# Kernel tuning notes

Hardware: AMD Instinct MI355X
Metric: run time of the kernel (lower is better)

The kernel has to match this reference:

```python
import jax, jax.numpy as jnp
import numpy as np

N_NODES = 5000
N_EDGES = 160000
HID = 64
NODE_F = 4
TASK_F = 4
BATCH = 512


def _glorot(key, shape):
    fan_in = shape[-1]
    return jax.random.normal(key, shape, dtype=jnp.float32) / jnp.sqrt(jnp.float32(fan_in))


def setup_inputs() -> dict:
    key = jax.random.key(0)
    ks = jax.random.split(key, 16)
    x = jax.random.normal(ks[0], (N_NODES, NODE_F), dtype=jnp.float32)
    edge_index = jax.random.randint(ks[1], (2, N_EDGES), 0, N_NODES, dtype=jnp.int64)
    task_feat = jax.random.normal(ks[2], (BATCH, TASK_F), dtype=jnp.float32)
    return {
        "x": x,
        "edge_index": edge_index,
        "task_feat": task_feat,
        # SAGEConv layer 1: out = lin_l(mean_neigh) + lin_r(x); lin_l has bias, lin_r (root) has no bias (PyG default)
        "Wl1": _glorot(ks[3], (HID, NODE_F)), "bl1": jnp.zeros((HID,), jnp.float32),
        "Wr1": _glorot(ks[4], (HID, NODE_F)),
        # SAGEConv layer 2
        "Wl2": _glorot(ks[5], (HID, HID)), "bl2": jnp.zeros((HID,), jnp.float32),
        "Wr2": _glorot(ks[6], (HID, HID)),
        # task_encoder: Linear(4,64) -> ReLU -> Linear(64,64)
        "Wt1": _glorot(ks[7], (HID, TASK_F)), "bt1": jnp.zeros((HID,), jnp.float32),
        "Wt2": _glorot(ks[8], (HID, HID)), "bt2": jnp.zeros((HID,), jnp.float32),
        # classifier: Linear(128,64) -> ReLU -> Linear(64,1)
        "Wc1": _glorot(ks[9], (HID, 2 * HID)), "bc1": jnp.zeros((HID,), jnp.float32),
        "Wc2": _glorot(ks[10], (1, HID)), "bc2": jnp.zeros((1,), jnp.float32),
    }


def _sage_conv(x, src, dst, Wl, bl, Wr):
    # PyG SAGEConv(mean): messages flow src -> dst; mean over incoming neighbors
    msg_sum = jax.ops.segment_sum(x[src], dst, num_segments=N_NODES)
    deg = jax.ops.segment_sum(jnp.ones((src.shape[0],), x.dtype), dst, num_segments=N_NODES)
    mean_neigh = msg_sum / jnp.maximum(deg, 1.0)[:, None]
    return mean_neigh @ Wl.T + bl + x @ Wr.T


def reference(x, edge_index, task_feat,
              Wl1, bl1, Wr1, Wl2, bl2, Wr2,
              Wt1, bt1, Wt2, bt2, Wc1, bc1, Wc2, bc2):
    src, dst = edge_index[0], edge_index[1]
    h = jax.nn.relu(_sage_conv(x, src, dst, Wl1, bl1, Wr1))        # [N, HID]
    h = jax.nn.relu(_sage_conv(h, src, dst, Wl2, bl2, Wr2))        # [N, HID]
    t = jax.nn.relu(task_feat @ Wt1.T + bt1) @ Wt2.T + bt2         # [B, HID]
    # classifier on concat([h, t]) == split Wc1 into h-part and t-part; avoids materializing the concat
    h_part = h @ Wc1[:, :HID].T                                    # [N, HID]
    t_part = t @ Wc1[:, HID:].T + bc1                              # [B, HID]
    hidden = jax.nn.relu(h_part[None, :, :] + t_part[:, None, :])  # [B, N, HID]
    scores = jnp.einsum('bnh,h->bn', hidden, Wc2[0]) + bc2[0]      # [B, N]
    return scores
```

## Files before the change

kernel.cpp:

```cpp
#include <hip/hip_runtime.h>

#define N_NODES 5000
#define N_EDGES 160000
#define HID 64
#define BATCH 512
#define EPB 2500
#define STRIDE 256


__global__ __launch_bounds__(256) void prep_kernel(
        const int* __restrict__ ei,
        const float* __restrict__ Wl1, const float* __restrict__ Wr1,
        const float* __restrict__ Wl2, const float* __restrict__ Wr2,
        const float* __restrict__ Wc1,
        const float* __restrict__ task_feat,
        const float* __restrict__ Wt1, const float* __restrict__ bt1,
        const float* __restrict__ Wt2, const float* __restrict__ bt2,
        const float* __restrict__ bc1,
        int* __restrict__ blk_hist,
        float* __restrict__ Wl1T, float* __restrict__ Wr1T,
        float* __restrict__ Wl2T, float* __restrict__ Wr2T,
        float* __restrict__ Wc1hT, float* __restrict__ t_part) {
    int tid = threadIdx.x;
    int blk = blockIdx.x;
    __shared__ int hist[N_NODES];
    __shared__ float s1[4][64], s2[4][64];

    if (blk < 64) {
        for (int i = tid; i < N_NODES; i += 256) hist[i] = 0;
        __syncthreads();
        int base = blk * EPB;
        for (int j = tid; j < EPB; j += 256)
            atomicAdd(&hist[ei[N_EDGES + base + j]], 1);
        __syncthreads();
        for (int i = tid; i < N_NODES; i += 256)
            blk_hist[blk * N_NODES + i] = hist[i];
    } else if (blk == 64) {
        for (int idx = tid; idx < 4096; idx += 256) {
            int k = idx >> 6, h = idx & 63;
            Wl2T[idx] = Wl2[h * 64 + k];
        }
    } else if (blk == 65) {
        for (int idx = tid; idx < 4096; idx += 256) {
            int k = idx >> 6, h = idx & 63;
            Wr2T[idx] = Wr2[h * 64 + k];
        }
    } else if (blk == 66) {
        for (int idx = tid; idx < 4096; idx += 256) {
            int k = idx >> 6, h = idx & 63;
            Wc1hT[idx] = Wc1[h * 128 + k];
        }
    } else if (blk == 67) {
        int k = tid >> 6, h = tid & 63;
        Wl1T[tid] = Wl1[h * 4 + k];
        Wr1T[tid] = Wr1[h * 4 + k];
    } else {
        int grp = tid >> 6, h = tid & 63;
        int b = (blk - 68) * 4 + grp;
        float4 tf = ((const float4*)task_feat)[b];
        float4 w1 = ((const float4*)Wt1)[h];
        float v = bt1[h] + tf.x * w1.x + tf.y * w1.y + tf.z * w1.z + tf.w * w1.w;
        s1[grp][h] = fmaxf(v, 0.f);
        __syncthreads();
        const float4* w2r = (const float4*)(Wt2 + h * 64);
        const float4* s1v = (const float4*)s1[grp];
        float v2 = bt2[h];
#pragma unroll
        for (int q = 0; q < 16; q++) {
            float4 w = w2r[q]; float4 s = s1v[q];
            v2 += s.x * w.x + s.y * w.y + s.z * w.z + s.w * w.w;
        }
        s2[grp][h] = v2;
        __syncthreads();
        const float4* wc  = (const float4*)(Wc1 + h * 128 + 64);
        const float4* s2v = (const float4*)s2[grp];
        float p = bc1[h];
#pragma unroll
        for (int q = 0; q < 16; q++) {
            float4 w = wc[q]; float4 s = s2v[q];
            p += s.x * w.x + s.y * w.y + s.z * w.z + s.w * w.w;
        }
        t_part[b * 64 + h] = p;
    }
}

__global__ __launch_bounds__(256) void offsets_kernel(int* __restrict__ blk_hist,
                                                      int* __restrict__ deg) {
    int n = blockIdx.x * 256 + threadIdx.x;
    if (n >= N_NODES) return;
    int run = 0;
#pragma unroll 8
    for (int b = 0; b < 64; b++) {
        int v = blk_hist[b * N_NODES + n];
        blk_hist[b * N_NODES + n] = run;
        run += v;
    }
    deg[n] = run;
}

__global__ __launch_bounds__(256) void reorder_kernel(
        const int* __restrict__ ei, const int* __restrict__ blk_hist,
        int* __restrict__ sorted_src) {
    __shared__ int cur[N_NODES];
    int tid = threadIdx.x;
    int blk = blockIdx.x;
    for (int i = tid; i < N_NODES; i += 256) cur[i] = 0;
    __syncthreads();
    int base = blk * EPB;
    const int* my_excl = blk_hist + blk * N_NODES;
    for (int j = tid; j < EPB; j += 256) {
        int src = ei[base + j];
        int dst = ei[N_EDGES + base + j];
        int local = atomicAdd(&cur[dst], 1);
        sorted_src[dst * STRIDE + my_excl[dst] + local] = src;
    }
}

__global__ __launch_bounds__(256) void layer1_kernel(
        const float* __restrict__ x, const int* __restrict__ deg,
        const int* __restrict__ sorted_src,
        const float* __restrict__ Wl1T, const float* __restrict__ bl1,
        const float* __restrict__ Wr1T, float* __restrict__ h1) {
    int lane = threadIdx.x & 63, grp = threadIdx.x >> 6;
    int n = blockIdx.x * 4 + grp;
    int d = deg[n];
    int f = lane & 3, g = lane >> 2;
    const int* bucket = sorted_src + n * STRIDE;
    float acc = 0.f;
    for (int j = g; j < d; j += 16) acc += x[bucket[j] * 4 + f];
    acc += __shfl_down(acc, 32);
    acc += __shfl_down(acc, 16);
    acc += __shfl_down(acc, 8);
    acc += __shfl_down(acc, 4);
    __shared__ float mean[4][4], xn[4][4];
    if (lane < 4) {
        mean[grp][lane] = acc / fmaxf((float)d, 1.f);
        xn[grp][lane] = x[n * 4 + lane];
    }
    __syncthreads();
    float v = bl1[lane];
#pragma unroll
    for (int ff = 0; ff < 4; ff++)
        v += mean[grp][ff] * Wl1T[ff * 64 + lane] + xn[grp][ff] * Wr1T[ff * 64 + lane];
    h1[n * 64 + lane] = fmaxf(v, 0.f);
}

__global__ __launch_bounds__(256) void layer2_kernel(
        const float* __restrict__ h1, const int* __restrict__ deg,
        const int* __restrict__ sorted_src,
        const float* __restrict__ Wl2T, const float* __restrict__ bl2,
        const float* __restrict__ Wr2T, const float* __restrict__ Wc1hT,
        float* __restrict__ h_part) {
    int h = threadIdx.x & 63, grp = threadIdx.x >> 6;
    int n = blockIdx.x * 4 + grp;
    int d = deg[n];
    const int* bucket = sorted_src + n * STRIDE;
    float a0 = 0.f, a1 = 0.f, a2 = 0.f, a3 = 0.f;
    int j = 0;
    for (; j + 4 <= d; j += 4) {
        int e0 = bucket[j], e1 = bucket[j + 1], e2 = bucket[j + 2], e3 = bucket[j + 3];
        a0 += h1[e0 * 64 + h];
        a1 += h1[e1 * 64 + h];
        a2 += h1[e2 * 64 + h];
        a3 += h1[e3 * 64 + h];
    }
    for (; j < d; j++) a0 += h1[bucket[j] * 64 + h];
    float m = (a0 + a1 + a2 + a3) / fmaxf((float)d, 1.f);

    __shared__ float shm[4][64], shh[4][64], shh2[4][64];
    shm[grp][h] = m;
    shh[grp][h] = h1[n * 64 + h];
    __syncthreads();
    float v = bl2[h];
#pragma unroll
    for (int k = 0; k < 64; k++)
        v += shm[grp][k] * Wl2T[k * 64 + h] + shh[grp][k] * Wr2T[k * 64 + h];
    shh2[grp][h] = fmaxf(v, 0.f);
    __syncthreads();
    float p = 0.f;
#pragma unroll
    for (int k = 0; k < 64; k++) p += shh2[grp][k] * Wc1hT[k * 64 + h];
    h_part[n * 64 + h] = p;
}

__global__ __launch_bounds__(256) void scores_kernel(
        const float* __restrict__ h_part, const float* __restrict__ t_part,
        const float* __restrict__ Wc2, const float* __restrict__ bc2,
        float* __restrict__ out) {
    int tid = threadIdx.x;
    int n = blockIdx.x * 256 + tid;
    bool valid = n < N_NODES;
    int nn = valid ? n : (N_NODES - 1);
    float hr[64];
    const float4* hp = (const float4*)(h_part + nn * 64);
#pragma unroll
    for (int i = 0; i < 16; i++) {
        float4 v = hp[i];
        hr[4 * i + 0] = v.x; hr[4 * i + 1] = v.y;
        hr[4 * i + 2] = v.z; hr[4 * i + 3] = v.w;
    }
    float b2 = bc2[0];
    int b0 = blockIdx.y * 16;
    for (int bb = 0; bb < 16; bb++) {
        const float* tp = t_part + (b0 + bb) * 64;
        float acc = 0.f;
#pragma unroll
        for (int h = 0; h < 64; h++)
            acc = fmaf(fmaxf(hr[h] + tp[h], 0.f), Wc2[h], acc);
        if (valid) out[(b0 + bb) * N_NODES + n] = acc + b2;
    }
}

extern "C" void kernel_launch(void* const* d_in, const int* in_sizes, int n_in,
                              void* d_out, int out_size, void* d_ws, size_t ws_size,
                              hipStream_t stream) {
    const float* x    = (const float*)d_in[0];
    const int*   ei   = (const int*)d_in[1];
    const float* task = (const float*)d_in[2];
    const float* Wl1  = (const float*)d_in[3];
    const float* bl1  = (const float*)d_in[4];
    const float* Wr1  = (const float*)d_in[5];
    const float* Wl2  = (const float*)d_in[6];
    const float* bl2  = (const float*)d_in[7];
    const float* Wr2  = (const float*)d_in[8];
    const float* Wt1  = (const float*)d_in[9];
    const float* bt1  = (const float*)d_in[10];
    const float* Wt2  = (const float*)d_in[11];
    const float* bt2  = (const float*)d_in[12];
    const float* Wc1  = (const float*)d_in[13];
    const float* bc1  = (const float*)d_in[14];
    const float* Wc2  = (const float*)d_in[15];
    const float* bc2  = (const float*)d_in[16];
    float* out = (float*)d_out;

    char* ws = (char*)d_ws;
    int*   blk_hist   = (int*)(ws + 0);
    int*   deg        = (int*)(ws + 1280000);
    int*   sorted_src = (int*)(ws + 1300000);
    float* h1         = (float*)(ws + 6420000);
    float* h_part     = (float*)(ws + 7700000);
    float* t_part     = (float*)(ws + 8980000);
    float* Wl1T  = (float*)(ws + 9111072);
    float* Wr1T  = (float*)(ws + 9112096);
    float* Wl2T  = (float*)(ws + 9113120);
    float* Wr2T  = (float*)(ws + 9129504);
    float* Wc1hT = (float*)(ws + 9145888);

    prep_kernel<<<68 + BATCH / 4, 256, 0, stream>>>(ei, Wl1, Wr1, Wl2, Wr2, Wc1,
                                                    task, Wt1, bt1, Wt2, bt2, bc1,
                                                    blk_hist, Wl1T, Wr1T, Wl2T, Wr2T,
                                                    Wc1hT, t_part);
    offsets_kernel<<<(N_NODES + 255) / 256, 256, 0, stream>>>(blk_hist, deg);
    reorder_kernel<<<64, 256, 0, stream>>>(ei, blk_hist, sorted_src);
    layer1_kernel<<<N_NODES / 4, 256, 0, stream>>>(x, deg, sorted_src, Wl1T, bl1, Wr1T, h1);
    layer2_kernel<<<N_NODES / 4, 256, 0, stream>>>(h1, deg, sorted_src, Wl2T, bl2, Wr2T,
                                                   Wc1hT, h_part);
    scores_kernel<<<dim3(20, 32), 256, 0, stream>>>(h_part, t_part, Wc2, bc2, out);
}
```

Baseline: 154.6 us.

## Fuse all stages into one cooperative persistent kernel with grid syncs

```diff
diff --git a/kernel.cpp b/kernel.cpp
--- a/kernel.cpp
+++ b/kernel.cpp
@@ -1,259 +1,263 @@
 #include <hip/hip_runtime.h>
+#include <hip/hip_cooperative_groups.h>
+
+namespace cg = cooperative_groups;
 
 #define N_NODES 5000
 #define N_EDGES 160000
 #define HID 64
 #define BATCH 512
-#define EPB 2500
+#define NSLICE 128
+#define EPB (N_EDGES / NSLICE)
 #define STRIDE 256
-
-
-__global__ __launch_bounds__(256) void prep_kernel(
-        const int* __restrict__ ei,
-        const float* __restrict__ Wl1, const float* __restrict__ Wr1,
-        const float* __restrict__ Wl2, const float* __restrict__ Wr2,
-        const float* __restrict__ Wc1,
-        const float* __restrict__ task_feat,
-        const float* __restrict__ Wt1, const float* __restrict__ bt1,
-        const float* __restrict__ Wt2, const float* __restrict__ bt2,
-        const float* __restrict__ bc1,
-        int* __restrict__ blk_hist,
-        float* __restrict__ Wl1T, float* __restrict__ Wr1T,
-        float* __restrict__ Wl2T, float* __restrict__ Wr2T,
-        float* __restrict__ Wc1hT, float* __restrict__ t_part) {
-    int tid = threadIdx.x;
-    int blk = blockIdx.x;
-    __shared__ int hist[N_NODES];
-    __shared__ float s1[4][64], s2[4][64];
-
-    if (blk < 64) {
-        for (int i = tid; i < N_NODES; i += 256) hist[i] = 0;
+#define MAXGRID 640
+
+
+struct Params {
+    const float *x; const int *ei; const float *task;
+    const float *Wl1, *bl1, *Wr1, *Wl2, *bl2, *Wr2;
+    const float *Wt1, *bt1, *Wt2, *bt2, *Wc1, *bc1, *Wc2, *bc2;
+    float *out;
+    int *blk_hist; int *deg; int *sorted_src;
+    float *h1, *h_part, *t_part;
+    float *Wl1T, *Wr1T, *Wl2T, *Wr2T, *Wc1hT;
+};
+
+__global__ __launch_bounds__(256, 2) void fused_kernel(Params p) {
+    cg::grid_group grid = cg::this_grid();
+    const int tid = threadIdx.x;
+    const int nblk = gridDim.x;
+    __shared__ union SM {
+        int   ldsi[N_NODES];
+        float s[3][4][64];
+    } sm;
+
+    for (int u = blockIdx.x; u < NSLICE + 4 + BATCH / 4; u += nblk) {
+        if (u < NSLICE) {
+            for (int i = tid; i < N_NODES; i += 256) sm.ldsi[i] = 0;
+            __syncthreads();
+            int base = u * EPB;
+            for (int j = tid; j < EPB; j += 256)
+                atomicAdd(&sm.ldsi[p.ei[N_EDGES + base + j]], 1);
+            __syncthreads();
+            for (int i = tid; i < N_NODES; i += 256)
+                p.blk_hist[u * N_NODES + i] = sm.ldsi[i];
+        } else if (u < NSLICE + 4) {
+            int w = u - NSLICE;
+            if (w == 0) {
+                for (int idx = tid; idx < 4096; idx += 256) {
+                    int k = idx >> 6, h = idx & 63;
+                    p.Wl2T[idx] = p.Wl2[h * 64 + k];
+                }
+            } else if (w == 1) {
+                for (int idx = tid; idx < 4096; idx += 256) {
+                    int k = idx >> 6, h = idx & 63;
+                    p.Wr2T[idx] = p.Wr2[h * 64 + k];
+                }
+            } else if (w == 2) {
+                for (int idx = tid; idx < 4096; idx += 256) {
+                    int k = idx >> 6, h = idx & 63;
+                    p.Wc1hT[idx] = p.Wc1[h * 128 + k];
+                }
+            } else {
+                int k = tid >> 6, h = tid & 63;
+                p.Wl1T[tid] = p.Wl1[h * 4 + k];
+                p.Wr1T[tid] = p.Wr1[h * 4 + k];
+            }
+        } else {
+            int grp = tid >> 6, h = tid & 63;
+            int b = (u - (NSLICE + 4)) * 4 + grp;
+            float4 tf = ((const float4*)p.task)[b];
+            float4 w1 = ((const float4*)p.Wt1)[h];
+            float v = p.bt1[h] + tf.x * w1.x + tf.y * w1.y + tf.z * w1.z + tf.w * w1.w;
+            sm.s[0][grp][h] = fmaxf(v, 0.f);
+            __syncthreads();
+            const float4* w2r = (const float4*)(p.Wt2 + h * 64);
+            const float4* s1v = (const float4*)sm.s[0][grp];
+            float v2 = p.bt2[h];
+#pragma unroll
+            for (int q = 0; q < 16; q++) {
+                float4 w = w2r[q]; float4 s = s1v[q];
+                v2 += s.x * w.x + s.y * w.y + s.z * w.z + s.w * w.w;
+            }
+            sm.s[1][grp][h] = v2;
+            __syncthreads();
+            const float4* wc  = (const float4*)(p.Wc1 + h * 128 + 64);
+            const float4* s2v = (const float4*)sm.s[1][grp];
+            float pr = p.bc1[h];
+#pragma unroll
+            for (int q = 0; q < 16; q++) {
+                float4 w = wc[q]; float4 s = s2v[q];
+                pr += s.x * w.x + s.y * w.y + s.z * w.z + s.w * w.w;
+            }
+            p.t_part[b * 64 + h] = pr;
+        }
         __syncthreads();
-        int base = blk * EPB;
-        for (int j = tid; j < EPB; j += 256)
-            atomicAdd(&hist[ei[N_EDGES + base + j]], 1);
+    }
+    grid.sync();
+
+    for (int n = blockIdx.x * 256 + tid; n < N_NODES; n += nblk * 256) {
+        int run = 0;
+#pragma unroll 8
+        for (int b = 0; b < NSLICE; b++) {
+            int v = p.blk_hist[b * N_NODES + n];
+            p.blk_hist[b * N_NODES + n] = run;
+            run += v;
+        }
+        p.deg[n] = run;
+    }
+    grid.sync();
+
+    for (int u = blockIdx.x; u < NSLICE; u += nblk) {
+        for (int i = tid; i < N_NODES; i += 256) sm.ldsi[i] = 0;
         __syncthreads();
-        for (int i = tid; i < N_NODES; i += 256)
-            blk_hist[blk * N_NODES + i] = hist[i];
-    } else if (blk == 64) {
-        for (int idx = tid; idx < 4096; idx += 256) {
-            int k = idx >> 6, h = idx & 63;
-            Wl2T[idx] = Wl2[h * 64 + k];
-        }
-    } else if (blk == 65) {
-        for (int idx = tid; idx < 4096; idx += 256) {
-            int k = idx >> 6, h = idx & 63;
-            Wr2T[idx] = Wr2[h * 64 + k];
-        }
-    } else if (blk == 66) {
-        for (int idx = tid; idx < 4096; idx += 256) {
-            int k = idx >> 6, h = idx & 63;
-            Wc1hT[idx] = Wc1[h * 128 + k];
-        }
-    } else if (blk == 67) {
-        int k = tid >> 6, h = tid & 63;
-        Wl1T[tid] = Wl1[h * 4 + k];
-        Wr1T[tid] = Wr1[h * 4 + k];
-    } else {
-        int grp = tid >> 6, h = tid & 63;
-        int b = (blk - 68) * 4 + grp;
-        float4 tf = ((const float4*)task_feat)[b];
-        float4 w1 = ((const float4*)Wt1)[h];
-        float v = bt1[h] + tf.x * w1.x + tf.y * w1.y + tf.z * w1.z + tf.w * w1.w;
-        s1[grp][h] = fmaxf(v, 0.f);
+        int base = u * EPB;
+        const int* excl = p.blk_hist + u * N_NODES;
+        for (int j = tid; j < EPB; j += 256) {
+            int src = p.ei[base + j];
+            int dst = p.ei[N_EDGES + base + j];
+            int local = atomicAdd(&sm.ldsi[dst], 1);
+            p.sorted_src[dst * STRIDE + excl[dst] + local] = src;
+        }
         __syncthreads();
-        const float4* w2r = (const float4*)(Wt2 + h * 64);
-        const float4* s1v = (const float4*)s1[grp];
-        float v2 = bt2[h];
-#pragma unroll
-        for (int q = 0; q < 16; q++) {
-            float4 w = w2r[q]; float4 s = s1v[q];
-            v2 += s.x * w.x + s.y * w.y + s.z * w.z + s.w * w.w;
-        }
-        s2[grp][h] = v2;
-        __syncthreads();
-        const float4* wc  = (const float4*)(Wc1 + h * 128 + 64);
-        const float4* s2v = (const float4*)s2[grp];
-        float p = bc1[h];
-#pragma unroll
-        for (int q = 0; q < 16; q++) {
-            float4 w = wc[q]; float4 s = s2v[q];
-            p += s.x * w.x + s.y * w.y + s.z * w.z + s.w * w.w;
-        }
-        t_part[b * 64 + h] = p;
-    }
-}
-
-__global__ __launch_bounds__(256) void offsets_kernel(int* __restrict__ blk_hist,
-                                                      int* __restrict__ deg) {
-    int n = blockIdx.x * 256 + threadIdx.x;
-    if (n >= N_NODES) return;
-    int run = 0;
-#pragma unroll 8
-    for (int b = 0; b < 64; b++) {
-        int v = blk_hist[b * N_NODES + n];
-        blk_hist[b * N_NODES + n] = run;
-        run += v;
-    }
-    deg[n] = run;
-}
-
-__global__ __launch_bounds__(256) void reorder_kernel(
-        const int* __restrict__ ei, const int* __restrict__ blk_hist,
-        int* __restrict__ sorted_src) {
-    __shared__ int cur[N_NODES];
-    int tid = threadIdx.x;
-    int blk = blockIdx.x;
-    for (int i = tid; i < N_NODES; i += 256) cur[i] = 0;
-    __syncthreads();
-    int base = blk * EPB;
-    const int* my_excl = blk_hist + blk * N_NODES;
-    for (int j = tid; j < EPB; j += 256) {
-        int src = ei[base + j];
-        int dst = ei[N_EDGES + base + j];
-        int local = atomicAdd(&cur[dst], 1);
-        sorted_src[dst * STRIDE + my_excl[dst] + local] = src;
-    }
-}
-
-__global__ __launch_bounds__(256) void layer1_kernel(
-        const float* __restrict__ x, const int* __restrict__ deg,
-        const int* __restrict__ sorted_src,
-        const float* __restrict__ Wl1T, const float* __restrict__ bl1,
-        const float* __restrict__ Wr1T, float* __restrict__ h1) {
-    int lane = threadIdx.x & 63, grp = threadIdx.x >> 6;
-    int n = blockIdx.x * 4 + grp;
-    int d = deg[n];
-    int f = lane & 3, g = lane >> 2;
-    const int* bucket = sorted_src + n * STRIDE;
-    float acc = 0.f;
-    for (int j = g; j < d; j += 16) acc += x[bucket[j] * 4 + f];
-    acc += __shfl_down(acc, 32);
-    acc += __shfl_down(acc, 16);
-    acc += __shfl_down(acc, 8);
-    acc += __shfl_down(acc, 4);
-    __shared__ float mean[4][4], xn[4][4];
-    if (lane < 4) {
-        mean[grp][lane] = acc / fmaxf((float)d, 1.f);
-        xn[grp][lane] = x[n * 4 + lane];
-    }
-    __syncthreads();
-    float v = bl1[lane];
-#pragma unroll
-    for (int ff = 0; ff < 4; ff++)
-        v += mean[grp][ff] * Wl1T[ff * 64 + lane] + xn[grp][ff] * Wr1T[ff * 64 + lane];
-    h1[n * 64 + lane] = fmaxf(v, 0.f);
-}
-
-__global__ __launch_bounds__(256) void layer2_kernel(
-        const float* __restrict__ h1, const int* __restrict__ deg,
-        const int* __restrict__ sorted_src,
-        const float* __restrict__ Wl2T, const float* __restrict__ bl2,
-        const float* __restrict__ Wr2T, const float* __restrict__ Wc1hT,
-        float* __restrict__ h_part) {
-    int h = threadIdx.x & 63, grp = threadIdx.x >> 6;
-    int n = blockIdx.x * 4 + grp;
-    int d = deg[n];
-    const int* bucket = sorted_src + n * STRIDE;
-    float a0 = 0.f, a1 = 0.f, a2 = 0.f, a3 = 0.f;
-    int j = 0;
-    for (; j + 4 <= d; j += 4) {
-        int e0 = bucket[j], e1 = bucket[j + 1], e2 = bucket[j + 2], e3 = bucket[j + 3];
-        a0 += h1[e0 * 64 + h];
-        a1 += h1[e1 * 64 + h];
-        a2 += h1[e2 * 64 + h];
-        a3 += h1[e3 * 64 + h];
-    }
-    for (; j < d; j++) a0 += h1[bucket[j] * 64 + h];
-    float m = (a0 + a1 + a2 + a3) / fmaxf((float)d, 1.f);
-
-    __shared__ float shm[4][64], shh[4][64], shh2[4][64];
-    shm[grp][h] = m;
-    shh[grp][h] = h1[n * 64 + h];
-    __syncthreads();
-    float v = bl2[h];
-#pragma unroll
-    for (int k = 0; k < 64; k++)
-        v += shm[grp][k] * Wl2T[k * 64 + h] + shh[grp][k] * Wr2T[k * 64 + h];
-    shh2[grp][h] = fmaxf(v, 0.f);
-    __syncthreads();
-    float p = 0.f;
-#pragma unroll
-    for (int k = 0; k < 64; k++) p += shh2[grp][k] * Wc1hT[k * 64 + h];
-    h_part[n * 64 + h] = p;
-}
-
-__global__ __launch_bounds__(256) void scores_kernel(
-        const float* __restrict__ h_part, const float* __restrict__ t_part,
-        const float* __restrict__ Wc2, const float* __restrict__ bc2,
-        float* __restrict__ out) {
-    int tid = threadIdx.x;
-    int n = blockIdx.x * 256 + tid;
-    bool valid = n < N_NODES;
-    int nn = valid ? n : (N_NODES - 1);
-    float hr[64];
-    const float4* hp = (const float4*)(h_part + nn * 64);
-#pragma unroll
-    for (int i = 0; i < 16; i++) {
-        float4 v = hp[i];
-        hr[4 * i + 0] = v.x; hr[4 * i + 1] = v.y;
-        hr[4 * i + 2] = v.z; hr[4 * i + 3] = v.w;
-    }
-    float b2 = bc2[0];
-    int b0 = blockIdx.y * 16;
-    for (int bb = 0; bb < 16; bb++) {
-        const float* tp = t_part + (b0 + bb) * 64;
-        float acc = 0.f;
-#pragma unroll
-        for (int h = 0; h < 64; h++)
-            acc = fmaf(fmaxf(hr[h] + tp[h], 0.f), Wc2[h], acc);
-        if (valid) out[(b0 + bb) * N_NODES + n] = acc + b2;
+    }
+    grid.sync();
+
+    {
+        int lane = tid & 63, grp = tid >> 6;
+        int f = lane & 3, g = lane >> 2;
+        for (int q = blockIdx.x; q < N_NODES / 4; q += nblk) {
+            int n = q * 4 + grp;
+            int d = p.deg[n];
+            const int* bucket = p.sorted_src + n * STRIDE;
+            float acc = 0.f;
+            for (int j = g; j < d; j += 16) acc += p.x[bucket[j] * 4 + f];
+            acc += __shfl_down(acc, 32);
+            acc += __shfl_down(acc, 16);
+            acc += __shfl_down(acc, 8);
+            acc += __shfl_down(acc, 4);
+            if (lane < 4) {
+                sm.s[0][grp][lane] = acc / fmaxf((float)d, 1.f);
+                sm.s[1][grp][lane] = p.x[n * 4 + lane];
+            }
+            __syncthreads();
+            float v = p.bl1[lane];
+#pragma unroll
+            for (int ff = 0; ff < 4; ff++)
+                v += sm.s[0][grp][ff] * p.Wl1T[ff * 64 + lane]
+                   + sm.s[1][grp][ff] * p.Wr1T[ff * 64 + lane];
+            p.h1[n * 64 + lane] = fmaxf(v, 0.f);
+            __syncthreads();
+        }
+    }
+    grid.sync();
+
+    {
+        int h = tid & 63, grp = tid >> 6;
+        for (int q = blockIdx.x; q < N_NODES / 4; q += nblk) {
+            int n = q * 4 + grp;
+            int d = p.deg[n];
+            const int* bucket = p.sorted_src + n * STRIDE;
+            float a0 = 0.f, a1 = 0.f, a2 = 0.f, a3 = 0.f;
+            int j = 0;
+            for (; j + 4 <= d; j += 4) {
+                int e0 = bucket[j], e1 = bucket[j + 1], e2 = bucket[j + 2], e3 = bucket[j + 3];
+                a0 += p.h1[e0 * 64 + h];
+                a1 += p.h1[e1 * 64 + h];
+                a2 += p.h1[e2 * 64 + h];
+                a3 += p.h1[e3 * 64 + h];
+            }
+            for (; j < d; j++) a0 += p.h1[bucket[j] * 64 + h];
+            float m = (a0 + a1 + a2 + a3) / fmaxf((float)d, 1.f);
+
+            sm.s[0][grp][h] = m;
+            sm.s[1][grp][h] = p.h1[n * 64 + h];
+            __syncthreads();
+            float v = p.bl2[h];
+#pragma unroll
+            for (int k = 0; k < 64; k++)
+                v += sm.s[0][grp][k] * p.Wl2T[k * 64 + h]
+                   + sm.s[1][grp][k] * p.Wr2T[k * 64 + h];
+            __syncthreads();
+            sm.s[2][grp][h] = fmaxf(v, 0.f);
+            __syncthreads();
+            float pr = 0.f;
+#pragma unroll
+            for (int k = 0; k < 64; k++) pr += sm.s[2][grp][k] * p.Wc1hT[k * 64 + h];
+            p.h_part[n * 64 + h] = pr;
+            __syncthreads();
+        }
+    }
+    grid.sync();
+
+    for (int u = blockIdx.x; u < 640; u += nblk) {
+        int nt = u % 20, bt = u / 20;
+        int n = nt * 256 + tid;
+        bool valid = n < N_NODES;
+        int nn = valid ? n : (N_NODES - 1);
+        float hr[64];
+        const float4* hp = (const float4*)(p.h_part + nn * 64);
+#pragma unroll
+        for (int i = 0; i < 16; i++) {
+            float4 v = hp[i];
+            hr[4 * i + 0] = v.x; hr[4 * i + 1] = v.y;
+            hr[4 * i + 2] = v.z; hr[4 * i + 3] = v.w;
+        }
+        float b2 = p.bc2[0];
+        int b0 = bt * 16;
+        for (int bb = 0; bb < 16; bb++) {
+            const float* tp = p.t_part + (b0 + bb) * 64;
+            float acc = 0.f;
+#pragma unroll
+            for (int h = 0; h < 64; h++)
+                acc = fmaf(fmaxf(hr[h] + tp[h], 0.f), p.Wc2[h], acc);
+            if (valid) p.out[(b0 + bb) * N_NODES + n] = acc + b2;
+        }
     }
 }
 
 extern "C" void kernel_launch(void* const* d_in, const int* in_sizes, int n_in,
                               void* d_out, int out_size, void* d_ws, size_t ws_size,
                               hipStream_t stream) {
-    const float* x    = (const float*)d_in[0];
-    const int*   ei   = (const int*)d_in[1];
-    const float* task = (const float*)d_in[2];
-    const float* Wl1  = (const float*)d_in[3];
-    const float* bl1  = (const float*)d_in[4];
-    const float* Wr1  = (const float*)d_in[5];
-    const float* Wl2  = (const float*)d_in[6];
-    const float* bl2  = (const float*)d_in[7];
-    const float* Wr2  = (const float*)d_in[8];
-    const float* Wt1  = (const float*)d_in[9];
-    const float* bt1  = (const float*)d_in[10];
-    const float* Wt2  = (const float*)d_in[11];
-    const float* bt2  = (const float*)d_in[12];
-    const float* Wc1  = (const float*)d_in[13];
-    const float* bc1  = (const float*)d_in[14];
-    const float* Wc2  = (const float*)d_in[15];
-    const float* bc2  = (const float*)d_in[16];
-    float* out = (float*)d_out;
-
     char* ws = (char*)d_ws;
-    int*   blk_hist   = (int*)(ws + 0);
-    int*   deg        = (int*)(ws + 1280000);
-    int*   sorted_src = (int*)(ws + 1300000);
-    float* h1         = (float*)(ws + 6420000);
-    float* h_part     = (float*)(ws + 7700000);
-    float* t_part     = (float*)(ws + 8980000);
-    float* Wl1T  = (float*)(ws + 9111072);
-    float* Wr1T  = (float*)(ws + 9112096);
-    float* Wl2T  = (float*)(ws + 9113120);
-    float* Wr2T  = (float*)(ws + 9129504);
-    float* Wc1hT = (float*)(ws + 9145888);
-
-    prep_kernel<<<68 + BATCH / 4, 256, 0, stream>>>(ei, Wl1, Wr1, Wl2, Wr2, Wc1,
-                                                    task, Wt1, bt1, Wt2, bt2, bc1,
-                                                    blk_hist, Wl1T, Wr1T, Wl2T, Wr2T,
-                                                    Wc1hT, t_part);
-    offsets_kernel<<<(N_NODES + 255) / 256, 256, 0, stream>>>(blk_hist, deg);
-    reorder_kernel<<<64, 256, 0, stream>>>(ei, blk_hist, sorted_src);
-    layer1_kernel<<<N_NODES / 4, 256, 0, stream>>>(x, deg, sorted_src, Wl1T, bl1, Wr1T, h1);
-    layer2_kernel<<<N_NODES / 4, 256, 0, stream>>>(h1, deg, sorted_src, Wl2T, bl2, Wr2T,
-                                                   Wc1hT, h_part);
-    scores_kernel<<<dim3(20, 32), 256, 0, stream>>>(h_part, t_part, Wc2, bc2, out);
+    Params p;
+    p.x    = (const float*)d_in[0];
+    p.ei   = (const int*)d_in[1];
+    p.task = (const float*)d_in[2];
+    p.Wl1  = (const float*)d_in[3];
+    p.bl1  = (const float*)d_in[4];
+    p.Wr1  = (const float*)d_in[5];
+    p.Wl2  = (const float*)d_in[6];
+    p.bl2  = (const float*)d_in[7];
+    p.Wr2  = (const float*)d_in[8];
+    p.Wt1  = (const float*)d_in[9];
+    p.bt1  = (const float*)d_in[10];
+    p.Wt2  = (const float*)d_in[11];
+    p.bt2  = (const float*)d_in[12];
+    p.Wc1  = (const float*)d_in[13];
+    p.bc1  = (const float*)d_in[14];
+    p.Wc2  = (const float*)d_in[15];
+    p.bc2  = (const float*)d_in[16];
+    p.out  = (float*)d_out;
+    p.blk_hist   = (int*)(ws + 0);
+    p.deg        = (int*)(ws + 2560000);
+    p.sorted_src = (int*)(ws + 2580000);
+    p.h1         = (float*)(ws + 7700000);
+    p.h_part     = (float*)(ws + 8980000);
+    p.t_part     = (float*)(ws + 10260000);
+    p.Wl1T  = (float*)(ws + 10391072);
+    p.Wr1T  = (float*)(ws + 10392096);
+    p.Wl2T  = (float*)(ws + 10393120);
+    p.Wr2T  = (float*)(ws + 10409504);
+    p.Wc1hT = (float*)(ws + 10425888);
+
+    int maxb = 0;
+    hipOccupancyMaxActiveBlocksPerMultiprocessor(&maxb, (const void*)fused_kernel, 256, 0);
+    if (maxb < 1) maxb = 1;
+    long long grid = (long long)maxb * 256;
+    if (grid > MAXGRID) grid = MAXGRID;
+
+    void* args[] = { (void*)&p };
+    hipLaunchCooperativeKernel((const void*)fused_kernel, dim3((unsigned)grid), dim3(256),
+                               args, 0, stream);
 }
```

Measured after the change: 464.4 us. 3x slower.
